# Performance work log

Measured on AMD Instinct MI355X. Metric: run time of the kernel, lower is better.

## Reference

```python
import jax, jax.numpy as jnp
import numpy as np

N, E = 50000, 1600000
IN_CH, HEADS, OUT_PER_HEAD = 128, 4, 32  # out_channels=128 // 4 heads
NEG_SLOPE = 0.2


def setup_inputs() -> dict:
    key = jax.random.key(0)
    ks = jax.random.split(key, 10)
    HC = HEADS * OUT_PER_HEAD
    glorot = lambda k, shape: jax.random.uniform(k, shape, jnp.float32, -1.0, 1.0) * jnp.sqrt(6.0 / (shape[0] + shape[-1]))
    return {
        "x": jax.random.normal(ks[0], (N, IN_CH), jnp.float32),
        "edge_index": jax.random.randint(ks[1], (2, E), 0, N),
        "edge_weight": jax.random.uniform(ks[2], (E,), jnp.float32),
        "Wl": glorot(ks[3], (IN_CH, HC)),
        "bl": jnp.zeros((HC,), jnp.float32),
        "Wr": glorot(ks[4], (IN_CH, HC)),
        "br": jnp.zeros((HC,), jnp.float32),
        "We": glorot(ks[5], (1, HC)),           # lin_edge, bias=False
        "att": glorot(ks[6], (HEADS, OUT_PER_HEAD)),
        "bias": jnp.zeros((HC,), jnp.float32),
    }


def reference(x, edge_index, edge_weight, Wl, bl, Wr, br, We, att, bias):
    n = x.shape[0]
    H, C = att.shape
    src, dst = edge_index[0], edge_index[1]
    # add_self_loops with fill_value='max': self-loop edge_attr = max incoming edge weight per node (0 if none)
    loop_attr = jax.ops.segment_max(edge_weight, dst, num_segments=n)
    loop_attr = jnp.where(jnp.isfinite(loop_attr), loop_attr, 0.0)
    loop = jnp.arange(n)
    src_f = jnp.concatenate([src, loop])
    dst_f = jnp.concatenate([dst, loop])
    ea_f = jnp.concatenate([edge_weight, loop_attr])[:, None]  # [E+N, 1]
    # GATv2: separate src/dst linear transforms
    x_l = (x @ Wl + bl).reshape(n, H, C)
    x_r = (x @ Wr + br).reshape(n, H, C)
    e = (ea_f @ We).reshape(-1, H, C)
    # per-edge message and attention score
    m = jax.nn.leaky_relu(x_l[src_f] + x_r[dst_f] + e, NEG_SLOPE)  # [E+N, H, C]
    alpha = jnp.einsum('ehc,hc->eh', m, att)
    # scatter-softmax over incoming edges per destination node
    amax = jax.ops.segment_max(alpha, dst_f, num_segments=n)
    amax = jnp.where(jnp.isfinite(amax), amax, 0.0)
    aexp = jnp.exp(alpha - amax[dst_f])
    asum = jax.ops.segment_sum(aexp, dst_f, num_segments=n)
    alpha = aexp / (asum[dst_f] + 1e-16)
    # weighted aggregate of source-transformed features
    out = jax.ops.segment_sum(x_l[src_f] * alpha[..., None], dst_f, num_segments=n)
    return out.reshape(n, H * C) + bias
```

## Files before the change

### kernel.cpp

```cpp
#include <hip/hip_runtime.h>
#include <cstdint>

#define NEG 0.2f
#define BSH 4
#define BNODES 16
#define CAP 768
#define EPT 3
#define SBSH 9
#define SBN 512
#define CCAP 18000
#define CCHUNK 3328
#define CEPT 13
#define FSLICE 8
#define LOG2E 1.44269504088896f

typedef __attribute__((ext_vector_type(8))) short short8v;
typedef __attribute__((ext_vector_type(4))) float f32x4;
typedef __attribute__((ext_vector_type(2))) float f32x2;

__device__ __forceinline__ unsigned short f2bf(float f) {
  unsigned u = __float_as_uint(f);
  return (unsigned short)((u + 0x7FFFu + ((u >> 16) & 1u)) >> 16);
}
__device__ __forceinline__ float bf2f(unsigned short h) {
  return __uint_as_float(((unsigned)h) << 16);
}

__global__ __launch_bounds__(256) void k_prep(const float* __restrict__ Wl,
    const float* __restrict__ Wr, const float* __restrict__ We,
    const float* __restrict__ att, unsigned short* __restrict__ WtB,
    float* __restrict__ qe) {
  int mat = blockIdx.x;
  const float* W = mat ? Wr : Wl;
  for (int i = threadIdx.x; i < 16384; i += 256) {
    int c = i >> 7, k = i & 127;
    WtB[mat * 16384 + c * 128 + k] = f2bf(W[k * 128 + c]);
  }
  if (mat == 0) {
    __shared__ float tmp[128];
    if (threadIdx.x < 128) tmp[threadIdx.x] = att[threadIdx.x] * We[threadIdx.x];
    __syncthreads();
    if (threadIdx.x < 4) {
      float s = 0.f;
      for (int c = 0; c < 32; ++c) s += tmp[threadIdx.x * 32 + c];
      qe[threadIdx.x] = 0.6f * LOG2E * s;
    }
  }
}

__global__ __launch_bounds__(256) void k_gemm(const float* __restrict__ x,
    const unsigned short* __restrict__ WtB, const float* __restrict__ att,
    const float* __restrict__ bl, const float* __restrict__ br,
    unsigned short* __restrict__ xlb, unsigned short* __restrict__ xrb,
    float* __restrict__ ql, float* __restrict__ qr, int n) {
  __shared__ __align__(16) unsigned short xs[64][136];
  __shared__ __align__(16) unsigned short Wt[128][136];
  int tid = threadIdx.x;
  int B0 = blockIdx.x * 64;
  for (int i = tid; i < 64 * 32; i += 256) {
    int r = i >> 5, c4 = (i & 31) * 4;
    ushort4 o = {0, 0, 0, 0};
    if (B0 + r < n) {
      float4 v = *(const float4*)(x + (size_t)(B0 + r) * 128 + c4);
      o = make_ushort4(f2bf(v.x), f2bf(v.y), f2bf(v.z), f2bf(v.w));
    }
    *(ushort4*)&xs[r][c4] = o;
  }
  int wv = tid >> 6, lane = tid & 63;
  int l15 = lane & 15, g = lane >> 4;
  int R0 = wv * 16;
  int row = B0 + R0 + l15;
  for (int mat = 0; mat < 2; ++mat) {
    __syncthreads();
    for (int i = tid; i < 128 * 32; i += 256) {
      int c = i >> 5, k4 = (i & 31) * 4;
      *(ushort4*)&Wt[c][k4] = *(const ushort4*)(WtB + (size_t)mat * 16384 + c * 128 + k4);
    }
    __syncthreads();
    f32x4 acc[8];
    #pragma unroll
    for (int t = 0; t < 8; ++t) acc[t] = {0.f, 0.f, 0.f, 0.f};
    #pragma unroll
    for (int kc = 0; kc < 4; ++kc) {
      int k0 = kc * 32 + g * 8;
      short8v b = *(const short8v*)&xs[R0 + l15][k0];
      #pragma unroll
      for (int t = 0; t < 8; ++t) {
        short8v a = *(const short8v*)&Wt[t * 16 + l15][k0];
        acc[t] = __builtin_amdgcn_mfma_f32_16x16x32_bf16(a, b, acc[t], 0, 0, 0);
      }
    }
    const float* bias = mat ? br : bl;
    unsigned short* yp = mat ? xrb : xlb;
    float* qdst = mat ? qr : ql;
    float qp[4] = {0.f, 0.f, 0.f, 0.f};
    if (row < n) {
      const float s06 = 0.6f * LOG2E;
      #pragma unroll
      for (int t = 0; t < 8; ++t) {
        int c0 = t * 16 + g * 4;
        float4 bv = *(const float4*)(bias + c0);
        float4 av = *(const float4*)(att + c0);
        ushort4 o = {f2bf(acc[t][0] + bv.x), f2bf(acc[t][1] + bv.y),
                     f2bf(acc[t][2] + bv.z), f2bf(acc[t][3] + bv.w)};
        *(ushort4*)(yp + (size_t)row * 128 + c0) = o;
        float dot = av.x * bf2f(o.x) + av.y * bf2f(o.y)
                  + av.z * bf2f(o.z) + av.w * bf2f(o.w);
        qp[t >> 1] += s06 * dot;
      }
    }
    #pragma unroll
    for (int h = 0; h < 4; ++h) {
      qp[h] += __shfl_xor(qp[h], 16);
      qp[h] += __shfl_xor(qp[h], 32);
    }
    if (row < n && g == 0)
      *(float4*)(qdst + (size_t)row * 4) = make_float4(qp[0], qp[1], qp[2], qp[3]);
  }
}

__global__ __launch_bounds__(256) void k_coarse(const int* __restrict__ eidx,
    const float* __restrict__ ew, unsigned* __restrict__ gsb,
    int2* __restrict__ csb, int E, int NSB) {
  __shared__ unsigned cnt[128];
  __shared__ unsigned base[128];
  int c0 = blockIdx.x * CCHUNK;
  int c1 = min(E, c0 + CCHUNK);
  if (c0 >= c1) return;
  for (int b = threadIdx.x; b < NSB; b += 256) cnt[b] = 0u;
  __syncthreads();
  unsigned dreg[CEPT];
  #pragma unroll
  for (int k = 0; k < CEPT; ++k) {
    int i = c0 + threadIdx.x + k * 256;
    unsigned d = 0u;
    if (i < c1) {
      d = (unsigned)eidx[E + i];
      atomicAdd(&cnt[d >> SBSH], 1u);
    }
    dreg[k] = d;
  }
  __syncthreads();
  for (int b = threadIdx.x; b < NSB; b += 256) {
    unsigned c = cnt[b];
    base[b] = c ? atomicAdd(&gsb[b], c) : 0u;
    cnt[b] = 0u;
  }
  __syncthreads();
  #pragma unroll
  for (int k = 0; k < CEPT; ++k) {
    int i = c0 + threadIdx.x + k * 256;
    if (i < c1) {
      unsigned d = dreg[k];
      unsigned b = d >> SBSH;
      unsigned slot = base[b] + atomicAdd(&cnt[b], 1u);
      if (slot < CCAP)
        csb[(size_t)b * CCAP + slot] =
            make_int2((eidx[i] << SBSH) | (int)(d & (SBN - 1)), __float_as_int(ew[i]));
    }
  }
}

__global__ __launch_bounds__(256) void k_fine(const unsigned* __restrict__ gsb,
    const int2* __restrict__ csb, int2* __restrict__ ebkt,
    unsigned* __restrict__ fcnt, int NB) {
  __shared__ unsigned cnt[32];
  __shared__ unsigned base[32];
  int sb = blockIdx.x / FSLICE;
  int sl = blockIdx.x % FSLICE;
  int ne = min((int)gsb[sb], CCAP);
  int chunk = (ne + FSLICE - 1) / FSLICE;
  int i0 = sl * chunk, i1 = min(ne, i0 + chunk);
  if (i0 >= i1) return;
  const int2* src = csb + (size_t)sb * CCAP;
  if (threadIdx.x < 32) cnt[threadIdx.x] = 0u;
  __syncthreads();
  for (int i = i0 + threadIdx.x; i < i1; i += 256)
    atomicAdd(&cnt[(src[i].x >> 4) & 31], 1u);
  __syncthreads();
  if (threadIdx.x < 32) {
    unsigned c = cnt[threadIdx.x];
    base[threadIdx.x] = c ? atomicAdd(&fcnt[sb * 32 + (int)threadIdx.x], c) : 0u;
    cnt[threadIdx.x] = 0u;
  }
  __syncthreads();
  for (int i = i0 + threadIdx.x; i < i1; i += 256) {
    int2 e = src[i];
    int fb = (e.x >> 4) & 31;
    unsigned slot = base[fb] + atomicAdd(&cnt[fb], 1u);
    if (slot < CAP) {
      int packed = ((e.x >> SBSH) << 4) | (e.x & 15);
      ebkt[(size_t)(sb * 32 + fb) * CAP + slot] = make_int2(packed, e.y);
    }
  }
}

__global__ __launch_bounds__(256) void k_agg(
    const unsigned* __restrict__ fcnt, const int2* __restrict__ ebkt,
    const unsigned short* __restrict__ xlb, const unsigned short* __restrict__ xrb,
    const float* __restrict__ ql, const float* __restrict__ qr,
    const float* __restrict__ qe, const float* __restrict__ We,
    const float* __restrict__ att, const float* __restrict__ bias,
    float* __restrict__ out, int n) {
  __shared__ int2 es[CAP];
  __shared__ unsigned rp[BNODES + 1];
  __shared__ unsigned cur[BNODES];
  __shared__ unsigned scnt[BNODES];
  int tid = threadIdx.x;
  int lane = tid & 63, wv = tid >> 6;
  int bkt = blockIdx.x;
  int ne = min((int)fcnt[bkt], CAP);
  const int2* srcp = ebkt + (size_t)bkt * CAP;
  if (tid < BNODES) scnt[tid] = 0u;
  __syncthreads();
  int2 er[EPT];
  #pragma unroll
  for (int k = 0; k < EPT; ++k) {
    int i = tid + k * 256;
    if (i < ne) {
      er[k] = srcp[i];
      atomicAdd(&scnt[er[k].x & (BNODES - 1)], 1u);
    }
  }
  __syncthreads();
  if (tid < 64) {
    unsigned s = (lane < BNODES) ? scnt[lane] : 0u;
    #pragma unroll
    for (int off = 1; off < BNODES; off <<= 1) {
      unsigned t = __shfl_up(s, off);
      if (lane >= off) s += t;
    }
    if (lane < BNODES) { rp[lane + 1] = s; cur[lane] = 0u; }
    if (lane == 0) rp[0] = 0u;
  }
  __syncthreads();
  #pragma unroll
  for (int k = 0; k < EPT; ++k) {
    int i = tid + k * 256;
    if (i < ne) {
      int dl = er[k].x & (BNODES - 1);
      unsigned slot = rp[dl] + atomicAdd(&cur[dl], 1u);
      es[slot] = make_int2(er[k].x >> BSH, er[k].y);
    }
  }
  __syncthreads();

  int g = lane >> 4;
  int l4 = lane & 15;
  int h = l4 >> 2;
  int ch0 = l4 * 8;
  f32x2 we2[4], at2[4];
  {
    const float s04 = 0.4f * LOG2E;
    #pragma unroll
    for (int p = 0; p < 4; ++p) {
      float2 w = *(const float2*)(We + ch0 + p * 2);
      float2 a = *(const float2*)(att + ch0 + p * 2);
      we2[p] = (f32x2){w.x, w.y};
      at2[p] = (f32x2){s04 * a.x, s04 * a.y};
    }
  }
  float qeh = qe[h];

  for (int dl = wv; dl < BNODES; dl += 4) {
    int d = (bkt << BSH) + dl;
    if (d >= n) break;
    int s0 = (int)rp[dl], s1 = (int)rp[dl + 1];
    uint4 xrq = *(const uint4*)(xrb + ((size_t)d << 7) + ch0);
    f32x2 xr2[4];
    xr2[0] = (f32x2){__uint_as_float(xrq.x << 16), __uint_as_float(xrq.x & 0xFFFF0000u)};
    xr2[1] = (f32x2){__uint_as_float(xrq.y << 16), __uint_as_float(xrq.y & 0xFFFF0000u)};
    xr2[2] = (f32x2){__uint_as_float(xrq.z << 16), __uint_as_float(xrq.z & 0xFFFF0000u)};
    xr2[3] = (f32x2){__uint_as_float(xrq.w << 16), __uint_as_float(xrq.w & 0xFFFF0000u)};
    float qrd = qr[(size_t)d * 4 + h];
    float den = 0.f, wmax = -INFINITY;
    f32x2 a2[4];
    a2[0] = a2[1] = a2[2] = a2[3] = (f32x2){0.f, 0.f};
    int idx = s0 + g;
    bool valid = idx < s1;
    int2 ev = make_int2(0, 0);
    uint4 xq = {0, 0, 0, 0};
    float qls = 0.f;
    if (valid) {
      ev = es[idx];
      xq = *(const uint4*)(xlb + ((size_t)ev.x << 7) + ch0);
      qls = ql[(size_t)ev.x * 4 + h];
    }
    for (int j = s0; j < s1; j += 4) {
      int idxn = j + 4 + g;
      bool vn = idxn < s1;
      int2 evn = ev; uint4 xqn = xq; float qln = qls;
      if (vn) {
        evn = es[idxn];
        xqn = *(const uint4*)(xlb + ((size_t)evn.x << 7) + ch0);
        qln = ql[(size_t)evn.x * 4 + h];
      }
      if (valid) {
        float w = __int_as_float(ev.y);
        wmax = fmaxf(wmax, w);
        f32x2 w2 = (f32x2){w, w};
        f32x2 x2[4];
        x2[0] = (f32x2){__uint_as_float(xq.x << 16), __uint_as_float(xq.x & 0xFFFF0000u)};
        x2[1] = (f32x2){__uint_as_float(xq.y << 16), __uint_as_float(xq.y & 0xFFFF0000u)};
        x2[2] = (f32x2){__uint_as_float(xq.z << 16), __uint_as_float(xq.z & 0xFFFF0000u)};
        x2[3] = (f32x2){__uint_as_float(xq.w << 16), __uint_as_float(xq.w & 0xFFFF0000u)};
        f32x2 nl2 = (f32x2){0.f, 0.f};
        #pragma unroll
        for (int p = 0; p < 4; ++p) {
          f32x2 t2 = __builtin_elementwise_fma(w2, we2[p], xr2[p]) + x2[p];
          nl2 = __builtin_elementwise_fma(at2[p], __builtin_elementwise_abs(t2), nl2);
        }
        float nl = nl2.x + nl2.y;
        nl += __shfl_xor(nl, 1);
        nl += __shfl_xor(nl, 2);
        float pe = __builtin_amdgcn_exp2f(qls + fmaf(w, qeh, qrd) + nl);
        den += pe;
        f32x2 pe2 = (f32x2){pe, pe};
        #pragma unroll
        for (int p = 0; p < 4; ++p)
          a2[p] = __builtin_elementwise_fma(pe2, x2[p], a2[p]);
      }
      ev = evn; xq = xqn; qls = qln; valid = vn;
    }
    #pragma unroll
    for (int mask = 16; mask <= 32; mask <<= 1) {
      den += __shfl_xor(den, mask);
      #pragma unroll
      for (int p = 0; p < 4; ++p) {
        a2[p].x += __shfl_xor(a2[p].x, mask);
        a2[p].y += __shfl_xor(a2[p].y, mask);
      }
      wmax = fmaxf(wmax, __shfl_xor(wmax, mask));
    }
    {
      float wl = (wmax > -INFINITY) ? wmax : 0.f;
      uint4 xq2 = *(const uint4*)(xlb + ((size_t)d << 7) + ch0);
      f32x2 w2 = (f32x2){wl, wl};
      f32x2 x2[4];
      x2[0] = (f32x2){__uint_as_float(xq2.x << 16), __uint_as_float(xq2.x & 0xFFFF0000u)};
      x2[1] = (f32x2){__uint_as_float(xq2.y << 16), __uint_as_float(xq2.y & 0xFFFF0000u)};
      x2[2] = (f32x2){__uint_as_float(xq2.z << 16), __uint_as_float(xq2.z & 0xFFFF0000u)};
      x2[3] = (f32x2){__uint_as_float(xq2.w << 16), __uint_as_float(xq2.w & 0xFFFF0000u)};
      f32x2 nl2 = (f32x2){0.f, 0.f};
      #pragma unroll
      for (int p = 0; p < 4; ++p) {
        f32x2 t2 = __builtin_elementwise_fma(w2, we2[p], xr2[p]) + x2[p];
        nl2 = __builtin_elementwise_fma(at2[p], __builtin_elementwise_abs(t2), nl2);
      }
      float nl = nl2.x + nl2.y;
      nl += __shfl_xor(nl, 1);
      nl += __shfl_xor(nl, 2);
      float qld = ql[(size_t)d * 4 + h];
      float pe = __builtin_amdgcn_exp2f(qld + fmaf(wl, qeh, qrd) + nl);
      den += pe;
      f32x2 pe2 = (f32x2){pe, pe};
      #pragma unroll
      for (int p = 0; p < 4; ++p)
        a2[p] = __builtin_elementwise_fma(pe2, x2[p], a2[p]);
    }
    if (g == 0) {
      float r = 1.0f / den;
      float4 bvA = *(const float4*)(bias + ch0);
      float4 bvB = *(const float4*)(bias + ch0 + 4);
      float* op = out + (size_t)d * 128 + ch0;
      float4 oA = {a2[0].x * r + bvA.x, a2[0].y * r + bvA.y,
                   a2[1].x * r + bvA.z, a2[1].y * r + bvA.w};
      float4 oB = {a2[2].x * r + bvB.x, a2[2].y * r + bvB.y,
                   a2[3].x * r + bvB.z, a2[3].y * r + bvB.w};
      *(float4*)op = oA;
      *(float4*)(op + 4) = oB;
    }
  }
}

extern "C" void kernel_launch(void* const* d_in, const int* in_sizes, int n_in,
                              void* d_out, int out_size, void* d_ws, size_t ws_size,
                              hipStream_t stream) {
  const float* x     = (const float*)d_in[0];
  const int*   eidx  = (const int*)d_in[1];
  const float* ew_in = (const float*)d_in[2];
  const float* Wl    = (const float*)d_in[3];
  const float* bl    = (const float*)d_in[4];
  const float* Wr    = (const float*)d_in[5];
  const float* br    = (const float*)d_in[6];
  const float* We    = (const float*)d_in[7];
  const float* att   = (const float*)d_in[8];
  const float* bias  = (const float*)d_in[9];
  float* out = (float*)d_out;

  const int N = in_sizes[0] / 128;
  const int E = in_sizes[2];
  const int NB = (N + BNODES - 1) >> BSH;
  const int NSB = (N + SBN - 1) >> SBSH;

  char* ws = (char*)d_ws;
  size_t off = 0;
  auto alloc = [&](size_t bytes) {
    void* p = ws + off;
    off = (off + bytes + 255) & ~(size_t)255;
    return p;
  };
  int2* ebkt = (int2*)alloc((size_t)NB * CAP * 8);
  size_t ov_start = off;
  unsigned short* xlb = (unsigned short*)alloc((size_t)N * 128 * 2);
  unsigned short* xrb = (unsigned short*)alloc((size_t)N * 128 * 2);
  int2* csb = (int2*)(ws + ov_start);
  unsigned short* WtB = (unsigned short*)alloc(2 * 16384 * 2);
  float* ql = (float*)alloc((size_t)N * 4 * 4);
  float* qr = (float*)alloc((size_t)N * 4 * 4);
  float* qe = (float*)alloc(4 * 4);
  unsigned* fcnt = (unsigned*)alloc((size_t)NB * 4);
  unsigned* gsb  = (unsigned*)alloc((size_t)NSB * 4);

  size_t z0 = (size_t)((char*)fcnt - ws);
  size_t z1 = (size_t)((char*)gsb - ws) + (size_t)NSB * 4;
  hipMemsetAsync(ws + z0, 0, z1 - z0, stream);

  k_prep<<<2, 256, 0, stream>>>(Wl, Wr, We, att, WtB, qe);

  int nblk = (E + CCHUNK - 1) / CCHUNK;
  k_coarse<<<nblk, 256, 0, stream>>>(eidx, ew_in, gsb, csb, E, NSB);

  k_fine<<<NSB * FSLICE, 256, 0, stream>>>(gsb, csb, ebkt, fcnt, NB);

  k_gemm<<<(N + 63) / 64, 256, 0, stream>>>(x, WtB, att, bl, br, xlb, xrb, ql, qr, N);

  k_agg<<<NB, 256, 0, stream>>>(fcnt, ebkt, xlb, xrb, ql, qr, qe, We, att, bias, out, N);
}
```

Baseline: 162.8 us.

## Merge coarse edge binning with GEMM in one launch; deepen agg prefetch

The coarse edge-binning kernel and the bf16 projection GEMM now run as one launch, with block index deciding the role, so the two independent stages overlap on the GPU. This needs a dedicated csb buffer instead of aliasing xlb/xrb, which adds workspace size. The aggregation loop's software prefetch goes from one to two edge iterations ahead, keeping more gather loads in flight at the cost of extra registers. Both changes target latency: launch gaps and idle compute units between stages, and stalls on the gathers.

```diff
diff --git a/kernel.cpp b/kernel.cpp
--- a/kernel.cpp
+++ b/kernel.cpp
@@ -48,15 +48,58 @@
   }
 }
 
-__global__ __launch_bounds__(256) void k_gemm(const float* __restrict__ x,
-    const unsigned short* __restrict__ WtB, const float* __restrict__ att,
-    const float* __restrict__ bl, const float* __restrict__ br,
-    unsigned short* __restrict__ xlb, unsigned short* __restrict__ xrb,
-    float* __restrict__ ql, float* __restrict__ qr, int n) {
+__global__ __launch_bounds__(256) void k_gc(
+    const int* __restrict__ eidx, const float* __restrict__ ew,
+    unsigned* __restrict__ gsb, int2* __restrict__ csb, int E, int NSB, int NC,
+    const float* __restrict__ x, const unsigned short* __restrict__ WtB,
+    const float* __restrict__ att, const float* __restrict__ bl,
+    const float* __restrict__ br, unsigned short* __restrict__ xlb,
+    unsigned short* __restrict__ xrb, float* __restrict__ ql,
+    float* __restrict__ qr, int n) {
   __shared__ __align__(16) unsigned short xs[64][136];
   __shared__ __align__(16) unsigned short Wt[128][136];
   int tid = threadIdx.x;
-  int B0 = blockIdx.x * 64;
+  if ((int)blockIdx.x < NC) {
+    unsigned* cnt = (unsigned*)&xs[0][0];
+    unsigned* base = cnt + 128;
+    int c0 = blockIdx.x * CCHUNK;
+    int c1 = min(E, c0 + CCHUNK);
+    if (c0 >= c1) return;
+    for (int b = tid; b < NSB; b += 256) cnt[b] = 0u;
+    __syncthreads();
+    unsigned dreg[CEPT];
+    #pragma unroll
+    for (int k = 0; k < CEPT; ++k) {
+      int i = c0 + tid + k * 256;
+      unsigned d = 0u;
+      if (i < c1) {
+        d = (unsigned)eidx[E + i];
+        atomicAdd(&cnt[d >> SBSH], 1u);
+      }
+      dreg[k] = d;
+    }
+    __syncthreads();
+    for (int b = tid; b < NSB; b += 256) {
+      unsigned c = cnt[b];
+      base[b] = c ? atomicAdd(&gsb[b], c) : 0u;
+      cnt[b] = 0u;
+    }
+    __syncthreads();
+    #pragma unroll
+    for (int k = 0; k < CEPT; ++k) {
+      int i = c0 + tid + k * 256;
+      if (i < c1) {
+        unsigned d = dreg[k];
+        unsigned b = d >> SBSH;
+        unsigned slot = base[b] + atomicAdd(&cnt[b], 1u);
+        if (slot < CCAP)
+          csb[(size_t)b * CCAP + slot] =
+              make_int2((eidx[i] << SBSH) | (int)(d & (SBN - 1)), __float_as_int(ew[i]));
+      }
+    }
+    return;
+  }
+  int B0 = ((int)blockIdx.x - NC) * 64;
   for (int i = tid; i < 64 * 32; i += 256) {
     int r = i >> 5, c4 = (i & 31) * 4;
     ushort4 o = {0, 0, 0, 0};
@@ -119,48 +162,6 @@
   }
 }
 
-__global__ __launch_bounds__(256) void k_coarse(const int* __restrict__ eidx,
-    const float* __restrict__ ew, unsigned* __restrict__ gsb,
-    int2* __restrict__ csb, int E, int NSB) {
-  __shared__ unsigned cnt[128];
-  __shared__ unsigned base[128];
-  int c0 = blockIdx.x * CCHUNK;
-  int c1 = min(E, c0 + CCHUNK);
-  if (c0 >= c1) return;
-  for (int b = threadIdx.x; b < NSB; b += 256) cnt[b] = 0u;
-  __syncthreads();
-  unsigned dreg[CEPT];
-  #pragma unroll
-  for (int k = 0; k < CEPT; ++k) {
-    int i = c0 + threadIdx.x + k * 256;
-    unsigned d = 0u;
-    if (i < c1) {
-      d = (unsigned)eidx[E + i];
-      atomicAdd(&cnt[d >> SBSH], 1u);
-    }
-    dreg[k] = d;
-  }
-  __syncthreads();
-  for (int b = threadIdx.x; b < NSB; b += 256) {
-    unsigned c = cnt[b];
-    base[b] = c ? atomicAdd(&gsb[b], c) : 0u;
-    cnt[b] = 0u;
-  }
-  __syncthreads();
-  #pragma unroll
-  for (int k = 0; k < CEPT; ++k) {
-    int i = c0 + threadIdx.x + k * 256;
-    if (i < c1) {
-      unsigned d = dreg[k];
-      unsigned b = d >> SBSH;
-      unsigned slot = base[b] + atomicAdd(&cnt[b], 1u);
-      if (slot < CCAP)
-        csb[(size_t)b * CCAP + slot] =
-            make_int2((eidx[i] << SBSH) | (int)(d & (SBN - 1)), __float_as_int(ew[i]));
-    }
-  }
-}
-
 __global__ __launch_bounds__(256) void k_fine(const unsigned* __restrict__ gsb,
     const int2* __restrict__ csb, int2* __restrict__ ebkt,
     unsigned* __restrict__ fcnt, int NB) {
@@ -276,34 +277,39 @@
     float den = 0.f, wmax = -INFINITY;
     f32x2 a2[4];
     a2[0] = a2[1] = a2[2] = a2[3] = (f32x2){0.f, 0.f};
-    int idx = s0 + g;
-    bool valid = idx < s1;
-    int2 ev = make_int2(0, 0);
-    uint4 xq = {0, 0, 0, 0};
-    float qls = 0.f;
-    if (valid) {
-      ev = es[idx];
-      xq = *(const uint4*)(xlb + ((size_t)ev.x << 7) + ch0);
-      qls = ql[(size_t)ev.x * 4 + h];
+    int i0 = s0 + g, i1 = s0 + 4 + g;
+    bool v0 = i0 < s1, v1 = i1 < s1;
+    int2 e0 = make_int2(0, 0), e1 = make_int2(0, 0);
+    uint4 q0 = {0, 0, 0, 0}, q1 = {0, 0, 0, 0};
+    float l0 = 0.f, l1 = 0.f;
+    if (v0) {
+      e0 = es[i0];
+      q0 = *(const uint4*)(xlb + ((size_t)e0.x << 7) + ch0);
+      l0 = ql[(size_t)e0.x * 4 + h];
+    }
+    if (v1) {
+      e1 = es[i1];
+      q1 = *(const uint4*)(xlb + ((size_t)e1.x << 7) + ch0);
+      l1 = ql[(size_t)e1.x * 4 + h];
     }
     for (int j = s0; j < s1; j += 4) {
-      int idxn = j + 4 + g;
-      bool vn = idxn < s1;
-      int2 evn = ev; uint4 xqn = xq; float qln = qls;
-      if (vn) {
-        evn = es[idxn];
-        xqn = *(const uint4*)(xlb + ((size_t)evn.x << 7) + ch0);
-        qln = ql[(size_t)evn.x * 4 + h];
-      }
-      if (valid) {
-        float w = __int_as_float(ev.y);
+      int i2 = j + 8 + g;
+      bool v2 = i2 < s1;
+      int2 e2 = e0; uint4 q2 = q0; float l2 = l0;
+      if (v2) {
+        e2 = es[i2];
+        q2 = *(const uint4*)(xlb + ((size_t)e2.x << 7) + ch0);
+        l2 = ql[(size_t)e2.x * 4 + h];
+      }
+      if (v0) {
+        float w = __int_as_float(e0.y);
         wmax = fmaxf(wmax, w);
         f32x2 w2 = (f32x2){w, w};
         f32x2 x2[4];
-        x2[0] = (f32x2){__uint_as_float(xq.x << 16), __uint_as_float(xq.x & 0xFFFF0000u)};
-        x2[1] = (f32x2){__uint_as_float(xq.y << 16), __uint_as_float(xq.y & 0xFFFF0000u)};
-        x2[2] = (f32x2){__uint_as_float(xq.z << 16), __uint_as_float(xq.z & 0xFFFF0000u)};
-        x2[3] = (f32x2){__uint_as_float(xq.w << 16), __uint_as_float(xq.w & 0xFFFF0000u)};
+        x2[0] = (f32x2){__uint_as_float(q0.x << 16), __uint_as_float(q0.x & 0xFFFF0000u)};
+        x2[1] = (f32x2){__uint_as_float(q0.y << 16), __uint_as_float(q0.y & 0xFFFF0000u)};
+        x2[2] = (f32x2){__uint_as_float(q0.z << 16), __uint_as_float(q0.z & 0xFFFF0000u)};
+        x2[3] = (f32x2){__uint_as_float(q0.w << 16), __uint_as_float(q0.w & 0xFFFF0000u)};
         f32x2 nl2 = (f32x2){0.f, 0.f};
         #pragma unroll
         for (int p = 0; p < 4; ++p) {
@@ -313,14 +319,15 @@
         float nl = nl2.x + nl2.y;
         nl += __shfl_xor(nl, 1);
         nl += __shfl_xor(nl, 2);
-        float pe = __builtin_amdgcn_exp2f(qls + fmaf(w, qeh, qrd) + nl);
+        float pe = __builtin_amdgcn_exp2f(l0 + fmaf(w, qeh, qrd) + nl);
         den += pe;
         f32x2 pe2 = (f32x2){pe, pe};
         #pragma unroll
         for (int p = 0; p < 4; ++p)
           a2[p] = __builtin_elementwise_fma(pe2, x2[p], a2[p]);
       }
-      ev = evn; xq = xqn; qls = qln; valid = vn;
+      e0 = e1; q0 = q1; l0 = l1; v0 = v1;
+      e1 = e2; q1 = q2; l1 = l2; v1 = v2;
     }
     #pragma unroll
     for (int mask = 16; mask <= 32; mask <<= 1) {
@@ -401,10 +408,9 @@
     return p;
   };
   int2* ebkt = (int2*)alloc((size_t)NB * CAP * 8);
-  size_t ov_start = off;
+  int2* csb  = (int2*)alloc((size_t)NSB * CCAP * 8);
   unsigned short* xlb = (unsigned short*)alloc((size_t)N * 128 * 2);
   unsigned short* xrb = (unsigned short*)alloc((size_t)N * 128 * 2);
-  int2* csb = (int2*)(ws + ov_start);
   unsigned short* WtB = (unsigned short*)alloc(2 * 16384 * 2);
   float* ql = (float*)alloc((size_t)N * 4 * 4);
   float* qr = (float*)alloc((size_t)N * 4 * 4);
@@ -418,12 +424,12 @@
 
   k_prep<<<2, 256, 0, stream>>>(Wl, Wr, We, att, WtB, qe);
 
-  int nblk = (E + CCHUNK - 1) / CCHUNK;
-  k_coarse<<<nblk, 256, 0, stream>>>(eidx, ew_in, gsb, csb, E, NSB);
+  int NC = (E + CCHUNK - 1) / CCHUNK;
+  int NG = (N + 63) / 64;
+  k_gc<<<NC + NG, 256, 0, stream>>>(eidx, ew_in, gsb, csb, E, NSB, NC,
+                                    x, WtB, att, bl, br, xlb, xrb, ql, qr, N);
 
   k_fine<<<NSB * FSLICE, 256, 0, stream>>>(gsb, csb, ebkt, fcnt, NB);
 
-  k_gemm<<<(N + 63) / 64, 256, 0, stream>>>(x, WtB, att, bl, br, xlb, xrb, ql, qr, N);
-
   k_agg<<<NB, 256, 0, stream>>>(fcnt, ebkt, xlb, xrb, ql, qr, qe, We, att, bias, out, N);
 }
```

Result: faster. 155.7 us (-4.4%).

## Fuse coarse edge binning with node GEMM into one launch; fold memset into prep

Applied to the files above, without the earlier changes.

Merges the coarse destination-binning kernel and the bf16 node-feature GEMM into a single kernel whose blocks split by index, so the two independent stages run concurrently on the GPU. The counter zeroing moves from hipMemsetAsync into k_prep. The coarse bucket buffer no longer aliases the xlb/xrb region, which costs extra workspace but lets both stages write without conflict. This saves two launches and fills idle CUs. The GEMM's large shared-memory footprint now applies to the binning blocks too, which may lower their occupancy.

```diff
diff --git a/kernel.cpp b/kernel.cpp
--- a/kernel.cpp
+++ b/kernel.cpp
@@ -29,9 +29,15 @@
 __global__ __launch_bounds__(256) void k_prep(const float* __restrict__ Wl,
     const float* __restrict__ Wr, const float* __restrict__ We,
     const float* __restrict__ att, unsigned short* __restrict__ WtB,
-    float* __restrict__ qe) {
+    float* __restrict__ qe, unsigned* __restrict__ fcnt, int NB,
+    unsigned* __restrict__ gsb, int NSB) {
   int mat = blockIdx.x;
   const float* W = mat ? Wr : Wl;
+  if (mat == 0) {
+    for (int i = threadIdx.x; i < NB; i += 256) fcnt[i] = 0u;
+  } else {
+    for (int i = threadIdx.x; i < NSB; i += 256) gsb[i] = 0u;
+  }
   for (int i = threadIdx.x; i < 16384; i += 256) {
     int c = i >> 7, k = i & 127;
     WtB[mat * 16384 + c * 128 + k] = f2bf(W[k * 128 + c]);
@@ -48,15 +54,58 @@
   }
 }
 
-__global__ __launch_bounds__(256) void k_gemm(const float* __restrict__ x,
-    const unsigned short* __restrict__ WtB, const float* __restrict__ att,
-    const float* __restrict__ bl, const float* __restrict__ br,
-    unsigned short* __restrict__ xlb, unsigned short* __restrict__ xrb,
-    float* __restrict__ ql, float* __restrict__ qr, int n) {
+__global__ __launch_bounds__(256) void k_gc(
+    const int* __restrict__ eidx, const float* __restrict__ ew,
+    unsigned* __restrict__ gsb, int2* __restrict__ csb, int E, int NSB, int NC,
+    const float* __restrict__ x, const unsigned short* __restrict__ WtB,
+    const float* __restrict__ att, const float* __restrict__ bl,
+    const float* __restrict__ br, unsigned short* __restrict__ xlb,
+    unsigned short* __restrict__ xrb, float* __restrict__ ql,
+    float* __restrict__ qr, int n) {
   __shared__ __align__(16) unsigned short xs[64][136];
   __shared__ __align__(16) unsigned short Wt[128][136];
   int tid = threadIdx.x;
-  int B0 = blockIdx.x * 64;
+  if ((int)blockIdx.x < NC) {
+    unsigned* cnt = (unsigned*)&xs[0][0];
+    unsigned* base = cnt + 128;
+    int c0 = blockIdx.x * CCHUNK;
+    int c1 = min(E, c0 + CCHUNK);
+    if (c0 >= c1) return;
+    for (int b = tid; b < NSB; b += 256) cnt[b] = 0u;
+    __syncthreads();
+    unsigned dreg[CEPT];
+    #pragma unroll
+    for (int k = 0; k < CEPT; ++k) {
+      int i = c0 + tid + k * 256;
+      unsigned d = 0u;
+      if (i < c1) {
+        d = (unsigned)eidx[E + i];
+        atomicAdd(&cnt[d >> SBSH], 1u);
+      }
+      dreg[k] = d;
+    }
+    __syncthreads();
+    for (int b = tid; b < NSB; b += 256) {
+      unsigned c = cnt[b];
+      base[b] = c ? atomicAdd(&gsb[b], c) : 0u;
+      cnt[b] = 0u;
+    }
+    __syncthreads();
+    #pragma unroll
+    for (int k = 0; k < CEPT; ++k) {
+      int i = c0 + tid + k * 256;
+      if (i < c1) {
+        unsigned d = dreg[k];
+        unsigned b = d >> SBSH;
+        unsigned slot = base[b] + atomicAdd(&cnt[b], 1u);
+        if (slot < CCAP)
+          csb[(size_t)b * CCAP + slot] =
+              make_int2((eidx[i] << SBSH) | (int)(d & (SBN - 1)), __float_as_int(ew[i]));
+      }
+    }
+    return;
+  }
+  int B0 = ((int)blockIdx.x - NC) * 64;
   for (int i = tid; i < 64 * 32; i += 256) {
     int r = i >> 5, c4 = (i & 31) * 4;
     ushort4 o = {0, 0, 0, 0};
@@ -116,48 +165,6 @@
     }
     if (row < n && g == 0)
       *(float4*)(qdst + (size_t)row * 4) = make_float4(qp[0], qp[1], qp[2], qp[3]);
-  }
-}
-
-__global__ __launch_bounds__(256) void k_coarse(const int* __restrict__ eidx,
-    const float* __restrict__ ew, unsigned* __restrict__ gsb,
-    int2* __restrict__ csb, int E, int NSB) {
-  __shared__ unsigned cnt[128];
-  __shared__ unsigned base[128];
-  int c0 = blockIdx.x * CCHUNK;
-  int c1 = min(E, c0 + CCHUNK);
-  if (c0 >= c1) return;
-  for (int b = threadIdx.x; b < NSB; b += 256) cnt[b] = 0u;
-  __syncthreads();
-  unsigned dreg[CEPT];
-  #pragma unroll
-  for (int k = 0; k < CEPT; ++k) {
-    int i = c0 + threadIdx.x + k * 256;
-    unsigned d = 0u;
-    if (i < c1) {
-      d = (unsigned)eidx[E + i];
-      atomicAdd(&cnt[d >> SBSH], 1u);
-    }
-    dreg[k] = d;
-  }
-  __syncthreads();
-  for (int b = threadIdx.x; b < NSB; b += 256) {
-    unsigned c = cnt[b];
-    base[b] = c ? atomicAdd(&gsb[b], c) : 0u;
-    cnt[b] = 0u;
-  }
-  __syncthreads();
-  #pragma unroll
-  for (int k = 0; k < CEPT; ++k) {
-    int i = c0 + threadIdx.x + k * 256;
-    if (i < c1) {
-      unsigned d = dreg[k];
-      unsigned b = d >> SBSH;
-      unsigned slot = base[b] + atomicAdd(&cnt[b], 1u);
-      if (slot < CCAP)
-        csb[(size_t)b * CCAP + slot] =
-            make_int2((eidx[i] << SBSH) | (int)(d & (SBN - 1)), __float_as_int(ew[i]));
-    }
   }
 }
 
@@ -401,10 +408,9 @@
     return p;
   };
   int2* ebkt = (int2*)alloc((size_t)NB * CAP * 8);
-  size_t ov_start = off;
+  int2* csb  = (int2*)alloc((size_t)NSB * CCAP * 8);
   unsigned short* xlb = (unsigned short*)alloc((size_t)N * 128 * 2);
   unsigned short* xrb = (unsigned short*)alloc((size_t)N * 128 * 2);
-  int2* csb = (int2*)(ws + ov_start);
   unsigned short* WtB = (unsigned short*)alloc(2 * 16384 * 2);
   float* ql = (float*)alloc((size_t)N * 4 * 4);
   float* qr = (float*)alloc((size_t)N * 4 * 4);
@@ -412,18 +418,14 @@
   unsigned* fcnt = (unsigned*)alloc((size_t)NB * 4);
   unsigned* gsb  = (unsigned*)alloc((size_t)NSB * 4);
 
-  size_t z0 = (size_t)((char*)fcnt - ws);
-  size_t z1 = (size_t)((char*)gsb - ws) + (size_t)NSB * 4;
-  hipMemsetAsync(ws + z0, 0, z1 - z0, stream);
-
-  k_prep<<<2, 256, 0, stream>>>(Wl, Wr, We, att, WtB, qe);
-
-  int nblk = (E + CCHUNK - 1) / CCHUNK;
-  k_coarse<<<nblk, 256, 0, stream>>>(eidx, ew_in, gsb, csb, E, NSB);
+  k_prep<<<2, 256, 0, stream>>>(Wl, Wr, We, att, WtB, qe, fcnt, NB, gsb, NSB);
+
+  int NC = (E + CCHUNK - 1) / CCHUNK;
+  int NG = (N + 63) / 64;
+  k_gc<<<NC + NG, 256, 0, stream>>>(eidx, ew_in, gsb, csb, E, NSB, NC,
+                                    x, WtB, att, bl, br, xlb, xrb, ql, qr, N);
 
   k_fine<<<NSB * FSLICE, 256, 0, stream>>>(gsb, csb, ebkt, fcnt, NB);
 
-  k_gemm<<<(N + 63) / 64, 256, 0, stream>>>(x, WtB, att, bl, br, xlb, xrb, ql, qr, N);
-
   k_agg<<<NB, 256, 0, stream>>>(fcnt, ebkt, xlb, xrb, ql, qr, qe, We, att, bias, out, N);
 }
```

Result: faster. 143.9 us, median of 2 (-11.6%).
